# Performance work log

Measured on AMD Instinct MI355X. Metric: run time of the kernel, lower is better.

## Reference

```python
import jax, jax.numpy as jnp
import numpy as np
from jax import lax

EPS = 1e-5
K = 2


def conv1x1(x, w, b):
    # x: [B,C,H,W], w: [O,C], b: [O]
    return jnp.einsum('bchw,oc->bohw', x, w) + b[None, :, None, None]


def bn(x, g, b, m, v):
    # eval-mode BatchNorm2d with running stats m, v
    scale = g * lax.rsqrt(v + EPS)
    return (x - m[None, :, None, None]) * scale[None, :, None, None] + b[None, :, None, None]


def mrconv_xj(x, k):
    # Max-relative aggregation: running max over shifted diffs along H then W.
    # torch.cat([x[..,-i:,:], x[..,:-i,:]], dim=2) == roll by i along that axis.
    H, W = x.shape[2], x.shape[3]

    def make_step(axis):
        def step(xj, s):
            return jnp.maximum(xj, x - jnp.roll(x, s, axis=axis)), None
        return step

    shifts_h = jnp.arange(1, (H - 1) // k + 1) * k  # k, 2k, ..., < H
    shifts_w = jnp.arange(1, (W - 1) // k + 1) * k
    xj, _ = lax.scan(make_step(2), jnp.zeros_like(x), shifts_h)
    xj, _ = lax.scan(make_step(3), xj, shifts_w)
    return xj


def setup_inputs() -> dict:
    key = jax.random.key(0)
    ks = jax.random.split(key, 24)
    dim = 96
    B, H, W = 16, 112, 112
    d2, d4 = 2 * dim, 4 * dim

    def r(k, sh, s=0.05):
        return jax.random.normal(k, sh, jnp.float32) * s

    return dict(
        x=jax.random.normal(ks[0], (B, dim, H, W), jnp.float32),
        # Grapher.fc1: Conv2d(dim,dim,1) + BN(dim)
        w1=r(ks[1], (dim, dim)), b1=r(ks[2], (dim,)),
        g1=1.0 + r(ks[3], (dim,)), be1=r(ks[4], (dim,)),
        m1=r(ks[5], (dim,)), v1=1.0 + 0.1 * jax.random.uniform(ks[6], (dim,)),
        # MRConv4d.nn: Conv2d(2*dim, 2*dim, 1) + BN(2*dim) + GELU
        wg=r(ks[7], (d2, d2)), bg=r(ks[8], (d2,)),
        gg=1.0 + r(ks[9], (d2,)), beg=r(ks[10], (d2,)),
        mg=r(ks[11], (d2,)), vg=1.0 + 0.1 * jax.random.uniform(ks[12], (d2,)),
        # Grapher.fc2: Conv2d(2*dim, dim, 1) + BN(dim)
        w2=r(ks[13], (dim, d2)), b2=r(ks[14], (dim,)),
        g2=1.0 + r(ks[15], (dim,)), be2=r(ks[16], (dim,)),
        m2=r(ks[17], (dim,)), v2=1.0 + 0.1 * jax.random.uniform(ks[18], (dim,)),
        # FFN: Conv2d(dim, 4*dim, 1) -> GELU -> Conv2d(4*dim, dim, 1)
        wf1=r(ks[19], (d4, dim)), bf1=r(ks[20], (d4,)),
        wf2=r(ks[21], (dim, d4)), bf2=r(ks[22], (dim,)),
    )


def reference(x, w1, b1, g1, be1, m1, v1,
              wg, bg, gg, beg, mg, vg,
              w2, b2, g2, be2, m2, v2,
              wf1, bf1, wf2, bf2):
    # Grapher
    shortcut = x
    h = bn(conv1x1(x, w1, b1), g1, be1, m1, v1)          # fc1
    xj = mrconv_xj(h, K)                                 # max-relative graph conv
    h = jnp.concatenate([h, xj], axis=1)                 # [B, 2*dim, H, W]
    h = jax.nn.gelu(bn(conv1x1(h, wg, bg), gg, beg, mg, vg), approximate=False)
    h = bn(conv1x1(h, w2, b2), g2, be2, m2, v2) + shortcut  # fc2 + residual
    # FFN
    h = conv1x1(jax.nn.gelu(conv1x1(h, wf1, bf1), approximate=False), wf2, bf2)
    return h
```

## Files before the change

kernel.cpp:

```cpp
#include <hip/hip_runtime.h>
#include <hip/hip_bf16.h>
#include <math.h>

#define EPSC 1e-5f

typedef __attribute__((ext_vector_type(8))) short bf16x8;
typedef __attribute__((ext_vector_type(4))) float f32x4;
typedef __attribute__((ext_vector_type(8))) unsigned short u16x8;

constexpr int Bn = 16, Cn = 96, Hn = 112, Wn = 112, HWn = Hn * Wn;
constexpr int NT = 64, TPI = HWn / NT;

#define MFMA16(a, b, c) __builtin_amdgcn_mfma_f32_16x16x32_bf16((a), (b), (c), 0, 0, 0)

__device__ __forceinline__ ushort f2bf(float f) {
    __hip_bfloat16 h = __float2bfloat16(f);
    return __builtin_bit_cast(ushort, h);
}
__device__ __forceinline__ float bf2f(ushort u) {
    return __builtin_bit_cast(float, (unsigned)u << 16);
}
__device__ __forceinline__ float gelu_f(float x) {
    float t = x * x;
    float z = x * fmaf(0.0713548162726f, t, 1.59576912161f);
    float e = __expf(-z);
    return __fdividef(x, 1.0f + e);
}

__global__ __launch_bounds__(256) void params_kernel(
    const float* __restrict__ b1, const float* __restrict__ g1, const float* __restrict__ be1,
    const float* __restrict__ m1, const float* __restrict__ v1,
    const float* __restrict__ bg, const float* __restrict__ gg, const float* __restrict__ beg,
    const float* __restrict__ mg, const float* __restrict__ vg,
    const float* __restrict__ b2, const float* __restrict__ g2, const float* __restrict__ be2,
    const float* __restrict__ m2, const float* __restrict__ v2,
    float* __restrict__ P)
{
    int t = threadIdx.x;
    if (t < 96) {
        float s = g1[t] * rsqrtf(v1[t] + EPSC);
        P[t]       = s;
        P[96 + t]  = (b1[t] - m1[t]) * s + be1[t];
        float s2 = g2[t] * rsqrtf(v2[t] + EPSC);
        P[576 + t] = s2;
        P[672 + t] = (b2[t] - m2[t]) * s2 + be2[t];
    }
    if (t < 192) {
        float s = gg[t] * rsqrtf(vg[t] + EPSC);
        P[192 + t] = s;
        P[384 + t] = (bg[t] - mg[t]) * s + beg[t];
    }
}

__global__ __launch_bounds__(256) void pack_kernel(
    const float* __restrict__ w1, const float* __restrict__ wg, const float* __restrict__ w2,
    const float* __restrict__ wf1, const float* __restrict__ wf2,
    ushort* __restrict__ dst)
{
    int idx = blockIdx.x * 256 + threadIdx.x;
    if (idx >= 138240) return;
    const float* src; int K, off;
    if      (idx <   9216) { src = w1;  K =  96; off = 0;      }
    else if (idx <  46080) { src = wg;  K = 192; off = 9216;   }
    else if (idx <  64512) { src = w2;  K = 192; off = 46080;  }
    else if (idx < 101376) { src = wf1; K =  96; off = 64512;  }
    else                   { src = wf2; K = 384; off = 101376; }
    int r = idx - off;
    int e = r & 7, lane = (r >> 3) & 63, tile = r >> 9;
    int KC = K / 32;
    int kc = tile % KC, mt = tile / KC;
    int row = mt * 16 + (lane & 15);
    int col = kc * 32 + (lane >> 4) * 8 + e;
    dst[idx] = f2bf(src[(size_t)row * K + col]);
}

__global__ __launch_bounds__(256) void mins_kernel(
    const ushort* __restrict__ h, float* __restrict__ rmin2, float* __restrict__ cmin2)
{
    __shared__ __align__(16) ushort sl[112 * 96];
    int bid = blockIdx.x;
    int b = bid / 224, rem = bid % 224, mode = rem / 112, line = rem % 112;
    int t = threadIdx.x;
    if (mode == 0) {
        const ushort* base = h + ((size_t)b * HWn + line * Wn) * Cn;
        for (int v = t; v < 1344; v += 256)
            *(u16x8*)&sl[v * 8] = *(const u16x8*)&base[v * 8];
    } else {
        for (int v = t; v < 1344; v += 256) {
            int i = v / 12, g = v % 12;
            *(u16x8*)&sl[(i * 12 + g) * 8] =
                *(const u16x8*)&h[((size_t)b * HWn + i * Wn + line) * Cn + g * 8];
        }
    }
    __syncthreads();
    if (t < 192) {
        int c = t % 96, p = t / 96;
        float m = 1e30f;
        #pragma unroll 8
        for (int n = 0; n < 56; ++n) m = fminf(m, bf2f(sl[(p + 2 * n) * 96 + c]));
        float* dst = (mode == 0) ? rmin2 : cmin2;
        dst[(((size_t)b * 112 + line) * 2 + p) * 96 + c] = m;
    }
}

__global__ __launch_bounds__(256) void fc1_kernel(
    const float* __restrict__ X, const ushort* __restrict__ w1p,
    const float* __restrict__ prm, ushort* __restrict__ hbuf)
{
    __shared__ __align__(16) ushort Hs[64 * 104];
    int bid = blockIdx.x, b = bid / TPI, hw0 = (bid % TPI) * NT;
    int t = threadIdx.x, lane = t & 63, wave = t >> 6;
    int wm = wave >> 1, wn = wave & 1, q = lane >> 4, sl = lane & 15;

    bf16x8 bfr[3][2];
    #pragma unroll
    for (int kc = 0; kc < 3; ++kc)
        #pragma unroll
        for (int nc = 0; nc < 2; ++nc) {
            int s = hw0 + wn * 32 + nc * 16 + sl;
            union { bf16x8 v; ushort u[8]; } f;
            #pragma unroll
            for (int e = 0; e < 8; ++e) {
                int c = kc * 32 + q * 8 + e;
                f.u[e] = f2bf(X[((size_t)b * Cn + c) * HWn + s]);
            }
            bfr[kc][nc] = f.v;
        }
    f32x4 acc[3][2] = {};
    #pragma unroll
    for (int kc = 0; kc < 3; ++kc)
        #pragma unroll
        for (int m = 0; m < 3; ++m) {
            bf16x8 af = *(const bf16x8*)&w1p[(((wm * 3 + m) * 3 + kc) * 64 + lane) * 8];
            acc[m][0] = MFMA16(af, bfr[kc][0], acc[m][0]);
            acc[m][1] = MFMA16(af, bfr[kc][1], acc[m][1]);
        }
    #pragma unroll
    for (int m = 0; m < 3; ++m) {
        int o0 = (wm * 3 + m) * 16 + q * 4;
        f32x4 a4 = *(const f32x4*)&prm[o0];
        f32x4 s4 = *(const f32x4*)&prm[96 + o0];
        #pragma unroll
        for (int nc = 0; nc < 2; ++nc) {
            int srow = wn * 32 + nc * 16 + sl;
            ushort4 pk;
            pk.x = f2bf(acc[m][nc][0] * a4[0] + s4[0]);
            pk.y = f2bf(acc[m][nc][1] * a4[1] + s4[1]);
            pk.z = f2bf(acc[m][nc][2] * a4[2] + s4[2]);
            pk.w = f2bf(acc[m][nc][3] * a4[3] + s4[3]);
            *(ushort4*)&Hs[srow * 104 + o0] = pk;
        }
    }
    __syncthreads();
    for (int v = t; v < 768; v += 256) {
        int s = v / 12, g = v % 12;
        *(u16x8*)&hbuf[((size_t)b * HWn + hw0 + s) * Cn + g * 8] = *(const u16x8*)&Hs[s * 104 + g * 8];
    }
}

__global__ __launch_bounds__(256) void grapher_kernel(
    const ushort* __restrict__ hbuf, const float* __restrict__ Xres,
    const ushort* __restrict__ wgp, const ushort* __restrict__ w2p,
    const float* __restrict__ prm,
    const float* __restrict__ cmin2, const float* __restrict__ rmin2,
    ushort* __restrict__ rbuf)
{
    __shared__ __align__(16) ushort Xs[64 * 200];
    __shared__ __align__(16) ushort Gs[64 * 200];
    int bid = blockIdx.x, b = bid / TPI, hw0 = (bid % TPI) * NT;
    int t = threadIdx.x, lane = t & 63, wave = t >> 6;
    int wm = wave >> 1, wn = wave & 1, q = lane >> 4, sl = lane & 15;

    for (int v = t; v < 768; v += 256) {
        int s = v / 12, g = v % 12;
        u16x8 hv = *(const u16x8*)&hbuf[((size_t)b * HWn + hw0 + s) * Cn + g * 8];
        *(u16x8*)&Xs[s * 200 + g * 8] = hv;
        int pos = hw0 + s, i = pos / Wn, j = pos - i * Wn;
        const float* cm = &cmin2[(((size_t)b * 112 + j) * 2 + (i & 1)) * 96 + g * 8];
        const float* rm = &rmin2[(((size_t)b * 112 + i) * 2 + (j & 1)) * 96 + g * 8];
        union { u16x8 v; ushort u[8]; } hh, xx;
        hh.v = hv;
        #pragma unroll
        for (int e = 0; e < 8; ++e) {
            float hf = bf2f(hh.u[e]);
            xx.u[e] = f2bf(fmaxf(hf - cm[e], hf - rm[e]));
        }
        *(u16x8*)&Xs[s * 200 + 96 + g * 8] = xx.v;
    }
    __syncthreads();

    f32x4 acc[6][2] = {};
    #pragma unroll
    for (int kc = 0; kc < 6; ++kc) {
        bf16x8 b0 = *(const bf16x8*)&Xs[(wn * 32 + sl) * 200 + kc * 32 + q * 8];
        bf16x8 b1 = *(const bf16x8*)&Xs[(wn * 32 + 16 + sl) * 200 + kc * 32 + q * 8];
        #pragma unroll
        for (int m = 0; m < 6; ++m) {
            bf16x8 af = *(const bf16x8*)&wgp[(((wm * 6 + m) * 6 + kc) * 64 + lane) * 8];
            acc[m][0] = MFMA16(af, b0, acc[m][0]);
            acc[m][1] = MFMA16(af, b1, acc[m][1]);
        }
    }
    #pragma unroll
    for (int m = 0; m < 6; ++m) {
        int o0 = (wm * 6 + m) * 16 + q * 4;
        f32x4 a4 = *(const f32x4*)&prm[192 + o0];
        f32x4 s4 = *(const f32x4*)&prm[384 + o0];
        #pragma unroll
        for (int nc = 0; nc < 2; ++nc) {
            int srow = wn * 32 + nc * 16 + sl;
            ushort4 pk;
            pk.x = f2bf(gelu_f(acc[m][nc][0] * a4[0] + s4[0]));
            pk.y = f2bf(gelu_f(acc[m][nc][1] * a4[1] + s4[1]));
            pk.z = f2bf(gelu_f(acc[m][nc][2] * a4[2] + s4[2]));
            pk.w = f2bf(gelu_f(acc[m][nc][3] * a4[3] + s4[3]));
            *(ushort4*)&Gs[srow * 200 + o0] = pk;
        }
    }
    __syncthreads();

    f32x4 acc2[3][2] = {};
    #pragma unroll
    for (int kc = 0; kc < 6; ++kc) {
        bf16x8 b0 = *(const bf16x8*)&Gs[(wn * 32 + sl) * 200 + kc * 32 + q * 8];
        bf16x8 b1 = *(const bf16x8*)&Gs[(wn * 32 + 16 + sl) * 200 + kc * 32 + q * 8];
        #pragma unroll
        for (int m = 0; m < 3; ++m) {
            bf16x8 af = *(const bf16x8*)&w2p[(((wm * 3 + m) * 6 + kc) * 64 + lane) * 8];
            acc2[m][0] = MFMA16(af, b0, acc2[m][0]);
            acc2[m][1] = MFMA16(af, b1, acc2[m][1]);
        }
    }
    #pragma unroll
    for (int m = 0; m < 3; ++m) {
        int o0 = (wm * 3 + m) * 16 + q * 4;
        f32x4 a4 = *(const f32x4*)&prm[576 + o0];
        f32x4 s4 = *(const f32x4*)&prm[672 + o0];
        #pragma unroll
        for (int nc = 0; nc < 2; ++nc) {
            int srow = wn * 32 + nc * 16 + sl, sgl = hw0 + srow;
            ushort4 pk;
            float r0 = acc2[m][nc][0] * a4[0] + s4[0] + Xres[((size_t)b * Cn + o0 + 0) * HWn + sgl];
            float r1 = acc2[m][nc][1] * a4[1] + s4[1] + Xres[((size_t)b * Cn + o0 + 1) * HWn + sgl];
            float r2 = acc2[m][nc][2] * a4[2] + s4[2] + Xres[((size_t)b * Cn + o0 + 2) * HWn + sgl];
            float r3 = acc2[m][nc][3] * a4[3] + s4[3] + Xres[((size_t)b * Cn + o0 + 3) * HWn + sgl];
            pk.x = f2bf(r0); pk.y = f2bf(r1); pk.z = f2bf(r2); pk.w = f2bf(r3);
            *(ushort4*)&Xs[srow * 200 + o0] = pk;
        }
    }
    __syncthreads();
    for (int v = t; v < 768; v += 256) {
        int s = v / 12, g = v % 12;
        *(u16x8*)&rbuf[((size_t)b * HWn + hw0 + s) * Cn + g * 8] = *(const u16x8*)&Xs[s * 200 + g * 8];
    }
}

__global__ __launch_bounds__(256) void ffn_kernel(
    const ushort* __restrict__ rbuf,
    const ushort* __restrict__ wf1p, const float* __restrict__ bf1,
    const ushort* __restrict__ wf2p, const float* __restrict__ bf2,
    float* __restrict__ Out)
{
    __shared__ __align__(16) ushort Rs[64 * 104];
    __shared__ __align__(16) ushort Mc[2][64 * 104];
    int bid = blockIdx.x, b = bid / TPI, hw0 = (bid % TPI) * NT;
    int t = threadIdx.x, lane = t & 63, wave = t >> 6;
    int wm = wave >> 1, wn = wave & 1, q = lane >> 4, sl = lane & 15;

    for (int v = t; v < 768; v += 256) {
        int s = v / 12, g = v % 12;
        *(u16x8*)&Rs[s * 104 + g * 8] = *(const u16x8*)&rbuf[((size_t)b * HWn + hw0 + s) * Cn + g * 8];
    }
    __syncthreads();

    bf16x8 rb[3][2];
    #pragma unroll
    for (int kc = 0; kc < 3; ++kc) {
        rb[kc][0] = *(const bf16x8*)&Rs[(wn * 32 + sl) * 104 + kc * 32 + q * 8];
        rb[kc][1] = *(const bf16x8*)&Rs[(wn * 32 + 16 + sl) * 104 + kc * 32 + q * 8];
    }

    f32x4 acc2[3][2] = {};
    for (int c = 0; c < 4; ++c) {
        f32x4 a1[3][2] = {};
        #pragma unroll
        for (int kc = 0; kc < 3; ++kc)
            #pragma unroll
            for (int m = 0; m < 3; ++m) {
                bf16x8 af = *(const bf16x8*)&wf1p[(((c * 6 + wm * 3 + m) * 3 + kc) * 64 + lane) * 8];
                a1[m][0] = MFMA16(af, rb[kc][0], a1[m][0]);
                a1[m][1] = MFMA16(af, rb[kc][1], a1[m][1]);
            }
        ushort* mc = (ushort*)Mc[c & 1];
        #pragma unroll
        for (int m = 0; m < 3; ++m) {
            int ol = (wm * 3 + m) * 16 + q * 4;
            f32x4 b4 = *(const f32x4*)&bf1[c * 96 + ol];
            #pragma unroll
            for (int nc = 0; nc < 2; ++nc) {
                int srow = wn * 32 + nc * 16 + sl;
                ushort4 pk;
                pk.x = f2bf(gelu_f(a1[m][nc][0] + b4[0]));
                pk.y = f2bf(gelu_f(a1[m][nc][1] + b4[1]));
                pk.z = f2bf(gelu_f(a1[m][nc][2] + b4[2]));
                pk.w = f2bf(gelu_f(a1[m][nc][3] + b4[3]));
                *(ushort4*)&mc[srow * 104 + ol] = pk;
            }
        }
        __syncthreads();
        #pragma unroll
        for (int kc = 0; kc < 3; ++kc) {
            bf16x8 m0 = *(const bf16x8*)&mc[(wn * 32 + sl) * 104 + kc * 32 + q * 8];
            bf16x8 m1 = *(const bf16x8*)&mc[(wn * 32 + 16 + sl) * 104 + kc * 32 + q * 8];
            #pragma unroll
            for (int m = 0; m < 3; ++m) {
                bf16x8 af = *(const bf16x8*)&wf2p[(((wm * 3 + m) * 12 + c * 3 + kc) * 64 + lane) * 8];
                acc2[m][0] = MFMA16(af, m0, acc2[m][0]);
                acc2[m][1] = MFMA16(af, m1, acc2[m][1]);
            }
        }
    }
    #pragma unroll
    for (int m = 0; m < 3; ++m) {
        int o0 = (wm * 3 + m) * 16 + q * 4;
        f32x4 b4 = *(const f32x4*)&bf2[o0];
        #pragma unroll
        for (int nc = 0; nc < 2; ++nc) {
            int sgl = hw0 + wn * 32 + nc * 16 + sl;
            Out[((size_t)b * Cn + o0 + 0) * HWn + sgl] = acc2[m][nc][0] + b4[0];
            Out[((size_t)b * Cn + o0 + 1) * HWn + sgl] = acc2[m][nc][1] + b4[1];
            Out[((size_t)b * Cn + o0 + 2) * HWn + sgl] = acc2[m][nc][2] + b4[2];
            Out[((size_t)b * Cn + o0 + 3) * HWn + sgl] = acc2[m][nc][3] + b4[3];
        }
    }
}

extern "C" void kernel_launch(void* const* d_in, const int* in_sizes, int n_in,
                              void* d_out, int out_size, void* d_ws, size_t ws_size,
                              hipStream_t stream) {
    (void)in_sizes; (void)n_in; (void)out_size; (void)ws_size;
    const float* x   = (const float*)d_in[0];
    const float* w1  = (const float*)d_in[1];
    const float* b1  = (const float*)d_in[2];
    const float* g1  = (const float*)d_in[3];
    const float* be1 = (const float*)d_in[4];
    const float* m1  = (const float*)d_in[5];
    const float* v1  = (const float*)d_in[6];
    const float* wg  = (const float*)d_in[7];
    const float* bg  = (const float*)d_in[8];
    const float* gg  = (const float*)d_in[9];
    const float* beg = (const float*)d_in[10];
    const float* mg  = (const float*)d_in[11];
    const float* vg  = (const float*)d_in[12];
    const float* w2  = (const float*)d_in[13];
    const float* b2  = (const float*)d_in[14];
    const float* g2  = (const float*)d_in[15];
    const float* be2 = (const float*)d_in[16];
    const float* m2  = (const float*)d_in[17];
    const float* v2  = (const float*)d_in[18];
    const float* wf1 = (const float*)d_in[19];
    const float* bf1 = (const float*)d_in[20];
    const float* wf2 = (const float*)d_in[21];
    const float* bf2 = (const float*)d_in[22];
    float* out = (float*)d_out;

    char* base = (char*)d_ws;
    const size_t H_BYTES   = (size_t)Bn * HWn * Cn * 2;
    const size_t MIN_BYTES = (size_t)Bn * 112 * 2 * 96 * 4;
    ushort* hbuf  = (ushort*)base;
    float*  rmin2 = (float*)(base + H_BYTES);
    float*  cmin2 = (float*)(base + H_BYTES + MIN_BYTES);
    float*  prm   = (float*)(base + H_BYTES + 2 * MIN_BYTES);
    ushort* wpack = (ushort*)(base + H_BYTES + 2 * MIN_BYTES + 3072);
    ushort* w1p  = wpack;
    ushort* wgp  = wpack + 9216;
    ushort* w2p  = wpack + 46080;
    ushort* wf1p = wpack + 64512;
    ushort* wf2p = wpack + 101376;

    params_kernel<<<dim3(1), dim3(256), 0, stream>>>(
        b1, g1, be1, m1, v1, bg, gg, beg, mg, vg, b2, g2, be2, m2, v2, prm);
    pack_kernel<<<dim3(540), dim3(256), 0, stream>>>(w1, wg, w2, wf1, wf2, wpack);

    dim3 grid(Bn * TPI), blk(256);
    fc1_kernel<<<grid, blk, 0, stream>>>(x, w1p, prm, hbuf);
    mins_kernel<<<dim3(Bn * 2 * 112), blk, 0, stream>>>(hbuf, rmin2, cmin2);
    grapher_kernel<<<grid, blk, 0, stream>>>(hbuf, x, wgp, w2p, prm, cmin2, rmin2, hbuf);
    ffn_kernel<<<grid, blk, 0, stream>>>(hbuf, wf1p, bf1, wf2p, bf2, out);
}
```

Measured before the change: 211.5 us.

## Fuse grapher and FFN into one register-resident kernel with permuted weight packing

Merges grapher_kernel and ffn_kernel into a single mega_kernel in which each wave owns 16 spatial positions. Intermediate activations stay in registers: the MFMA accumulator outputs are repacked directly as B operands for the next matmul instead of going through LDS. To make that work, the w2, wf1 and wf2 packing is permuted along K so it matches the accumulator register layout. This removes the rbuf global round trip, the LDS staging and the __syncthreads, at the cost of more register pressure and per-wave reloading of the full weight fragments from global/L2, with launch_bounds set to 4 blocks.

```diff
diff --git a/kernel.cpp b/kernel.cpp
--- a/kernel.cpp
+++ b/kernel.cpp
@@ -25,6 +25,9 @@
     float z = x * fmaf(0.0713548162726f, t, 1.59576912161f);
     float e = __expf(-z);
     return __fdividef(x, 1.0f + e);
+}
+__device__ __forceinline__ uint pk2(float lo, float hi) {
+    return (uint)f2bf(lo) | ((uint)f2bf(hi) << 16);
 }
 
 __global__ __launch_bounds__(256) void params_kernel(
@@ -59,18 +62,20 @@
 {
     int idx = blockIdx.x * 256 + threadIdx.x;
     if (idx >= 138240) return;
-    const float* src; int K, off;
-    if      (idx <   9216) { src = w1;  K =  96; off = 0;      }
-    else if (idx <  46080) { src = wg;  K = 192; off = 9216;   }
-    else if (idx <  64512) { src = w2;  K = 192; off = 46080;  }
-    else if (idx < 101376) { src = wf1; K =  96; off = 64512;  }
-    else                   { src = wf2; K = 384; off = 101376; }
+    const float* src; int K, off; bool perm;
+    if      (idx <   9216) { src = w1;  K =  96; off = 0;      perm = false; }
+    else if (idx <  46080) { src = wg;  K = 192; off = 9216;   perm = false; }
+    else if (idx <  64512) { src = w2;  K = 192; off = 46080;  perm = true;  }
+    else if (idx < 101376) { src = wf1; K =  96; off = 64512;  perm = true;  }
+    else                   { src = wf2; K = 384; off = 101376; perm = true;  }
     int r = idx - off;
     int e = r & 7, lane = (r >> 3) & 63, tile = r >> 9;
     int KC = K / 32;
     int kc = tile % KC, mt = tile / KC;
     int row = mt * 16 + (lane & 15);
-    int col = kc * 32 + (lane >> 4) * 8 + e;
+    int col;
+    if (!perm) col = kc * 32 + (lane >> 4) * 8 + e;
+    else       col = ((kc >> 1) * 4 + (kc & 1) * 2 + (e >> 2)) * 16 + (lane >> 4) * 4 + (e & 3);
     dst[idx] = f2bf(src[(size_t)row * K + col]);
 }
 
@@ -158,180 +163,136 @@
     }
 }
 
-__global__ __launch_bounds__(256) void grapher_kernel(
+__global__ __launch_bounds__(256, 4) void mega_kernel(
     const ushort* __restrict__ hbuf, const float* __restrict__ Xres,
     const ushort* __restrict__ wgp, const ushort* __restrict__ w2p,
-    const float* __restrict__ prm,
+    const ushort* __restrict__ wf1p, const ushort* __restrict__ wf2p,
+    const float* __restrict__ prm, const float* __restrict__ bf1,
+    const float* __restrict__ bf2,
     const float* __restrict__ cmin2, const float* __restrict__ rmin2,
-    ushort* __restrict__ rbuf)
-{
-    __shared__ __align__(16) ushort Xs[64 * 200];
-    __shared__ __align__(16) ushort Gs[64 * 200];
+    float* __restrict__ Out)
+{
     int bid = blockIdx.x, b = bid / TPI, hw0 = (bid % TPI) * NT;
-    int t = threadIdx.x, lane = t & 63, wave = t >> 6;
-    int wm = wave >> 1, wn = wave & 1, q = lane >> 4, sl = lane & 15;
-
-    for (int v = t; v < 768; v += 256) {
-        int s = v / 12, g = v % 12;
-        u16x8 hv = *(const u16x8*)&hbuf[((size_t)b * HWn + hw0 + s) * Cn + g * 8];
-        *(u16x8*)&Xs[s * 200 + g * 8] = hv;
-        int pos = hw0 + s, i = pos / Wn, j = pos - i * Wn;
-        const float* cm = &cmin2[(((size_t)b * 112 + j) * 2 + (i & 1)) * 96 + g * 8];
-        const float* rm = &rmin2[(((size_t)b * 112 + i) * 2 + (j & 1)) * 96 + g * 8];
-        union { u16x8 v; ushort u[8]; } hh, xx;
-        hh.v = hv;
-        #pragma unroll
-        for (int e = 0; e < 8; ++e) {
-            float hf = bf2f(hh.u[e]);
-            xx.u[e] = f2bf(fmaxf(hf - cm[e], hf - rm[e]));
-        }
-        *(u16x8*)&Xs[s * 200 + 96 + g * 8] = xx.v;
-    }
-    __syncthreads();
-
-    f32x4 acc[6][2] = {};
+    int t = threadIdx.x, lane = t & 63, wv = t >> 6, q = lane >> 4, sl = lane & 15;
+    const int s = hw0 + wv * 16 + sl;
+    const int i = s / Wn, j = s - i * Wn;
+
+    union U8 { bf16x8 v; ushort u[8]; uint d[4]; };
+    const ushort* hrow = hbuf + ((size_t)b * HWn + s) * 96;
+    const size_t cmb = (((size_t)b * 112 + j) * 2 + (i & 1)) * 96;
+    const size_t rmb = (((size_t)b * 112 + i) * 2 + (j & 1)) * 96;
+
+    U8 cb[6];
+    #pragma unroll
+    for (int kc = 0; kc < 3; ++kc)
+        cb[kc].v = *(const bf16x8*)&hrow[kc * 32 + q * 8];
+    #pragma unroll
+    for (int kc = 0; kc < 3; ++kc) {
+        int c0 = kc * 32 + q * 8;
+        f32x4 cma = *(const f32x4*)&cmin2[cmb + c0];
+        f32x4 cmb2 = *(const f32x4*)&cmin2[cmb + c0 + 4];
+        f32x4 rma = *(const f32x4*)&rmin2[rmb + c0];
+        f32x4 rmb2 = *(const f32x4*)&rmin2[rmb + c0 + 4];
+        U8 xx;
+        #pragma unroll
+        for (int e = 0; e < 4; ++e) {
+            float hf = bf2f(cb[kc].u[e]);
+            xx.u[e] = f2bf(fmaxf(hf - cma[e], hf - rma[e]));
+        }
+        #pragma unroll
+        for (int e = 0; e < 4; ++e) {
+            float hf = bf2f(cb[kc].u[4 + e]);
+            xx.u[4 + e] = f2bf(fmaxf(hf - cmb2[e], hf - rmb2[e]));
+        }
+        cb[3 + kc] = xx;
+    }
+
+    f32x4 ga[12] = {};
+    #pragma unroll
+    for (int kc = 0; kc < 6; ++kc)
+        #pragma unroll
+        for (int m = 0; m < 12; ++m) {
+            bf16x8 af = *(const bf16x8*)&wgp[((m * 6 + kc) * 64 + lane) * 8];
+            ga[m] = MFMA16(af, cb[kc].v, ga[m]);
+        }
+    uint gpk[12][2];
+    #pragma unroll
+    for (int m = 0; m < 12; ++m) {
+        int t0 = m * 16 + q * 4;
+        f32x4 a4 = *(const f32x4*)&prm[192 + t0];
+        f32x4 s4 = *(const f32x4*)&prm[384 + t0];
+        gpk[m][0] = pk2(gelu_f(ga[m][0] * a4[0] + s4[0]), gelu_f(ga[m][1] * a4[1] + s4[1]));
+        gpk[m][1] = pk2(gelu_f(ga[m][2] * a4[2] + s4[2]), gelu_f(ga[m][3] * a4[3] + s4[3]));
+    }
+
+    f32x4 r2[6] = {};
     #pragma unroll
     for (int kc = 0; kc < 6; ++kc) {
-        bf16x8 b0 = *(const bf16x8*)&Xs[(wn * 32 + sl) * 200 + kc * 32 + q * 8];
-        bf16x8 b1 = *(const bf16x8*)&Xs[(wn * 32 + 16 + sl) * 200 + kc * 32 + q * 8];
+        int M = (kc >> 1) * 4 + (kc & 1) * 2;
+        U8 gb;
+        gb.d[0] = gpk[M][0];     gb.d[1] = gpk[M][1];
+        gb.d[2] = gpk[M + 1][0]; gb.d[3] = gpk[M + 1][1];
         #pragma unroll
         for (int m = 0; m < 6; ++m) {
-            bf16x8 af = *(const bf16x8*)&wgp[(((wm * 6 + m) * 6 + kc) * 64 + lane) * 8];
-            acc[m][0] = MFMA16(af, b0, acc[m][0]);
-            acc[m][1] = MFMA16(af, b1, acc[m][1]);
-        }
-    }
+            bf16x8 af = *(const bf16x8*)&w2p[((m * 6 + kc) * 64 + lane) * 8];
+            r2[m] = MFMA16(af, gb.v, r2[m]);
+        }
+    }
+    uint rpk[6][2];
     #pragma unroll
     for (int m = 0; m < 6; ++m) {
-        int o0 = (wm * 6 + m) * 16 + q * 4;
-        f32x4 a4 = *(const f32x4*)&prm[192 + o0];
-        f32x4 s4 = *(const f32x4*)&prm[384 + o0];
-        #pragma unroll
-        for (int nc = 0; nc < 2; ++nc) {
-            int srow = wn * 32 + nc * 16 + sl;
-            ushort4 pk;
-            pk.x = f2bf(gelu_f(acc[m][nc][0] * a4[0] + s4[0]));
-            pk.y = f2bf(gelu_f(acc[m][nc][1] * a4[1] + s4[1]));
-            pk.z = f2bf(gelu_f(acc[m][nc][2] * a4[2] + s4[2]));
-            pk.w = f2bf(gelu_f(acc[m][nc][3] * a4[3] + s4[3]));
-            *(ushort4*)&Gs[srow * 200 + o0] = pk;
-        }
-    }
-    __syncthreads();
-
-    f32x4 acc2[3][2] = {};
-    #pragma unroll
-    for (int kc = 0; kc < 6; ++kc) {
-        bf16x8 b0 = *(const bf16x8*)&Gs[(wn * 32 + sl) * 200 + kc * 32 + q * 8];
-        bf16x8 b1 = *(const bf16x8*)&Gs[(wn * 32 + 16 + sl) * 200 + kc * 32 + q * 8];
-        #pragma unroll
-        for (int m = 0; m < 3; ++m) {
-            bf16x8 af = *(const bf16x8*)&w2p[(((wm * 3 + m) * 6 + kc) * 64 + lane) * 8];
-            acc2[m][0] = MFMA16(af, b0, acc2[m][0]);
-            acc2[m][1] = MFMA16(af, b1, acc2[m][1]);
-        }
-    }
-    #pragma unroll
-    for (int m = 0; m < 3; ++m) {
-        int o0 = (wm * 3 + m) * 16 + q * 4;
-        f32x4 a4 = *(const f32x4*)&prm[576 + o0];
-        f32x4 s4 = *(const f32x4*)&prm[672 + o0];
-        #pragma unroll
-        for (int nc = 0; nc < 2; ++nc) {
-            int srow = wn * 32 + nc * 16 + sl, sgl = hw0 + srow;
-            ushort4 pk;
-            float r0 = acc2[m][nc][0] * a4[0] + s4[0] + Xres[((size_t)b * Cn + o0 + 0) * HWn + sgl];
-            float r1 = acc2[m][nc][1] * a4[1] + s4[1] + Xres[((size_t)b * Cn + o0 + 1) * HWn + sgl];
-            float r2 = acc2[m][nc][2] * a4[2] + s4[2] + Xres[((size_t)b * Cn + o0 + 2) * HWn + sgl];
-            float r3 = acc2[m][nc][3] * a4[3] + s4[3] + Xres[((size_t)b * Cn + o0 + 3) * HWn + sgl];
-            pk.x = f2bf(r0); pk.y = f2bf(r1); pk.z = f2bf(r2); pk.w = f2bf(r3);
-            *(ushort4*)&Xs[srow * 200 + o0] = pk;
-        }
-    }
-    __syncthreads();
-    for (int v = t; v < 768; v += 256) {
-        int s = v / 12, g = v % 12;
-        *(u16x8*)&rbuf[((size_t)b * HWn + hw0 + s) * Cn + g * 8] = *(const u16x8*)&Xs[s * 200 + g * 8];
-    }
-}
-
-__global__ __launch_bounds__(256) void ffn_kernel(
-    const ushort* __restrict__ rbuf,
-    const ushort* __restrict__ wf1p, const float* __restrict__ bf1,
-    const ushort* __restrict__ wf2p, const float* __restrict__ bf2,
-    float* __restrict__ Out)
-{
-    __shared__ __align__(16) ushort Rs[64 * 104];
-    __shared__ __align__(16) ushort Mc[2][64 * 104];
-    int bid = blockIdx.x, b = bid / TPI, hw0 = (bid % TPI) * NT;
-    int t = threadIdx.x, lane = t & 63, wave = t >> 6;
-    int wm = wave >> 1, wn = wave & 1, q = lane >> 4, sl = lane & 15;
-
-    for (int v = t; v < 768; v += 256) {
-        int s = v / 12, g = v % 12;
-        *(u16x8*)&Rs[s * 104 + g * 8] = *(const u16x8*)&rbuf[((size_t)b * HWn + hw0 + s) * Cn + g * 8];
-    }
-    __syncthreads();
-
-    bf16x8 rb[3][2];
+        int t0 = m * 16 + q * 4;
+        f32x4 a4 = *(const f32x4*)&prm[576 + t0];
+        f32x4 s4 = *(const f32x4*)&prm[672 + t0];
+        float rv[4];
+        #pragma unroll
+        for (int r = 0; r < 4; ++r)
+            rv[r] = r2[m][r] * a4[r] + s4[r] + Xres[((size_t)b * 96 + t0 + r) * HWn + s];
+        rpk[m][0] = pk2(rv[0], rv[1]);
+        rpk[m][1] = pk2(rv[2], rv[3]);
+    }
+    U8 rB[3];
     #pragma unroll
     for (int kc = 0; kc < 3; ++kc) {
-        rb[kc][0] = *(const bf16x8*)&Rs[(wn * 32 + sl) * 104 + kc * 32 + q * 8];
-        rb[kc][1] = *(const bf16x8*)&Rs[(wn * 32 + 16 + sl) * 104 + kc * 32 + q * 8];
-    }
-
-    f32x4 acc2[3][2] = {};
-    for (int c = 0; c < 4; ++c) {
-        f32x4 a1[3][2] = {};
+        rB[kc].d[0] = rpk[kc * 2][0];     rB[kc].d[1] = rpk[kc * 2][1];
+        rB[kc].d[2] = rpk[kc * 2 + 1][0]; rB[kc].d[3] = rpk[kc * 2 + 1][1];
+    }
+
+    f32x4 oacc[6] = {};
+    for (int c = 0; c < 6; ++c) {
+        f32x4 a1[4] = {};
         #pragma unroll
         for (int kc = 0; kc < 3; ++kc)
             #pragma unroll
-            for (int m = 0; m < 3; ++m) {
-                bf16x8 af = *(const bf16x8*)&wf1p[(((c * 6 + wm * 3 + m) * 3 + kc) * 64 + lane) * 8];
-                a1[m][0] = MFMA16(af, rb[kc][0], a1[m][0]);
-                a1[m][1] = MFMA16(af, rb[kc][1], a1[m][1]);
+            for (int m = 0; m < 4; ++m) {
+                bf16x8 af = *(const bf16x8*)&wf1p[(((c * 4 + m) * 3 + kc) * 64 + lane) * 8];
+                a1[m] = MFMA16(af, rB[kc].v, a1[m]);
             }
-        ushort* mc = (ushort*)Mc[c & 1];
-        #pragma unroll
-        for (int m = 0; m < 3; ++m) {
-            int ol = (wm * 3 + m) * 16 + q * 4;
-            f32x4 b4 = *(const f32x4*)&bf1[c * 96 + ol];
-            #pragma unroll
-            for (int nc = 0; nc < 2; ++nc) {
-                int srow = wn * 32 + nc * 16 + sl;
-                ushort4 pk;
-                pk.x = f2bf(gelu_f(a1[m][nc][0] + b4[0]));
-                pk.y = f2bf(gelu_f(a1[m][nc][1] + b4[1]));
-                pk.z = f2bf(gelu_f(a1[m][nc][2] + b4[2]));
-                pk.w = f2bf(gelu_f(a1[m][nc][3] + b4[3]));
-                *(ushort4*)&mc[srow * 104 + ol] = pk;
-            }
-        }
-        __syncthreads();
-        #pragma unroll
-        for (int kc = 0; kc < 3; ++kc) {
-            bf16x8 m0 = *(const bf16x8*)&mc[(wn * 32 + sl) * 104 + kc * 32 + q * 8];
-            bf16x8 m1 = *(const bf16x8*)&mc[(wn * 32 + 16 + sl) * 104 + kc * 32 + q * 8];
-            #pragma unroll
-            for (int m = 0; m < 3; ++m) {
-                bf16x8 af = *(const bf16x8*)&wf2p[(((wm * 3 + m) * 12 + c * 3 + kc) * 64 + lane) * 8];
-                acc2[m][0] = MFMA16(af, m0, acc2[m][0]);
-                acc2[m][1] = MFMA16(af, m1, acc2[m][1]);
-            }
-        }
-    }
-    #pragma unroll
-    for (int m = 0; m < 3; ++m) {
-        int o0 = (wm * 3 + m) * 16 + q * 4;
-        f32x4 b4 = *(const f32x4*)&bf2[o0];
-        #pragma unroll
-        for (int nc = 0; nc < 2; ++nc) {
-            int sgl = hw0 + wn * 32 + nc * 16 + sl;
-            Out[((size_t)b * Cn + o0 + 0) * HWn + sgl] = acc2[m][nc][0] + b4[0];
-            Out[((size_t)b * Cn + o0 + 1) * HWn + sgl] = acc2[m][nc][1] + b4[1];
-            Out[((size_t)b * Cn + o0 + 2) * HWn + sgl] = acc2[m][nc][2] + b4[2];
-            Out[((size_t)b * Cn + o0 + 3) * HWn + sgl] = acc2[m][nc][3] + b4[3];
-        }
+        uint mpk[4][2];
+        #pragma unroll
+        for (int m = 0; m < 4; ++m) {
+            f32x4 b4 = *(const f32x4*)&bf1[(c * 4 + m) * 16 + q * 4];
+            mpk[m][0] = pk2(gelu_f(a1[m][0] + b4[0]), gelu_f(a1[m][1] + b4[1]));
+            mpk[m][1] = pk2(gelu_f(a1[m][2] + b4[2]), gelu_f(a1[m][3] + b4[3]));
+        }
+        U8 mB0, mB1;
+        mB0.d[0] = mpk[0][0]; mB0.d[1] = mpk[0][1]; mB0.d[2] = mpk[1][0]; mB0.d[3] = mpk[1][1];
+        mB1.d[0] = mpk[2][0]; mB1.d[1] = mpk[2][1]; mB1.d[2] = mpk[3][0]; mB1.d[3] = mpk[3][1];
+        #pragma unroll
+        for (int m = 0; m < 6; ++m) {
+            bf16x8 af0 = *(const bf16x8*)&wf2p[((m * 12 + c * 2) * 64 + lane) * 8];
+            oacc[m] = MFMA16(af0, mB0.v, oacc[m]);
+            bf16x8 af1 = *(const bf16x8*)&wf2p[((m * 12 + c * 2 + 1) * 64 + lane) * 8];
+            oacc[m] = MFMA16(af1, mB1.v, oacc[m]);
+        }
+    }
+    #pragma unroll
+    for (int m = 0; m < 6; ++m) {
+        int t0 = m * 16 + q * 4;
+        f32x4 b4 = *(const f32x4*)&bf2[t0];
+        #pragma unroll
+        for (int r = 0; r < 4; ++r)
+            Out[((size_t)b * 96 + t0 + r) * HWn + s] = oacc[m][r] + b4[r];
     }
 }
 
@@ -385,6 +346,6 @@
     dim3 grid(Bn * TPI), blk(256);
     fc1_kernel<<<grid, blk, 0, stream>>>(x, w1p, prm, hbuf);
     mins_kernel<<<dim3(Bn * 2 * 112), blk, 0, stream>>>(hbuf, rmin2, cmin2);
-    grapher_kernel<<<grid, blk, 0, stream>>>(hbuf, x, wgp, w2p, prm, cmin2, rmin2, hbuf);
-    ffn_kernel<<<grid, blk, 0, stream>>>(hbuf, wf1p, bf1, wf2p, bf2, out);
-}
+    mega_kernel<<<grid, blk, 0, stream>>>(hbuf, x, wgp, w2p, wf1p, wf2p,
+                                          prm, bf1, bf2, cmin2, rmin2, out);
+}
```

Result: slower. 309.9 us (+46.5%).

## Fuse grapher and FFN kernels into one tail kernel sharing LDS

Applied to the files above, without the earlier changes.

Merges the grapher kernel (graph conv, fc2 and residual) and the FFN kernel into a single kernel. The residual tile stays in shared memory and feeds the FFN directly instead of going to global memory as bf16 and being reloaded. Shared memory is reused: Xs holds the residual and Gs is split into the FFN double buffers. This saves one launch and a full activation write plus read, but raises per-block register pressure and lengthens the kernel.

```diff
diff --git a/kernel.cpp b/kernel.cpp
--- a/kernel.cpp
+++ b/kernel.cpp
@@ -158,15 +158,19 @@
     }
 }
 
-__global__ __launch_bounds__(256) void grapher_kernel(
+__global__ __launch_bounds__(256) void tail_kernel(
     const ushort* __restrict__ hbuf, const float* __restrict__ Xres,
     const ushort* __restrict__ wgp, const ushort* __restrict__ w2p,
+    const ushort* __restrict__ wf1p, const float* __restrict__ bf1,
+    const ushort* __restrict__ wf2p, const float* __restrict__ bf2,
     const float* __restrict__ prm,
     const float* __restrict__ cmin2, const float* __restrict__ rmin2,
-    ushort* __restrict__ rbuf)
-{
-    __shared__ __align__(16) ushort Xs[64 * 200];
-    __shared__ __align__(16) ushort Gs[64 * 200];
+    float* __restrict__ Out)
+{
+    __shared__ __align__(16) ushort S[26112];
+    ushort* Xs = S;
+    ushort* Gs = S + 12800;
+
     int bid = blockIdx.x, b = bid / TPI, hw0 = (bid % TPI) * NT;
     int t = threadIdx.x, lane = t & 63, wave = t >> 6;
     int wm = wave >> 1, wn = wave & 1, q = lane >> 4, sl = lane & 15;
@@ -189,95 +193,76 @@
     }
     __syncthreads();
 
-    f32x4 acc[6][2] = {};
-    #pragma unroll
-    for (int kc = 0; kc < 6; ++kc) {
-        bf16x8 b0 = *(const bf16x8*)&Xs[(wn * 32 + sl) * 200 + kc * 32 + q * 8];
-        bf16x8 b1 = *(const bf16x8*)&Xs[(wn * 32 + 16 + sl) * 200 + kc * 32 + q * 8];
+    {
+        f32x4 acc[6][2] = {};
+        #pragma unroll
+        for (int kc = 0; kc < 6; ++kc) {
+            bf16x8 b0 = *(const bf16x8*)&Xs[(wn * 32 + sl) * 200 + kc * 32 + q * 8];
+            bf16x8 b1 = *(const bf16x8*)&Xs[(wn * 32 + 16 + sl) * 200 + kc * 32 + q * 8];
+            #pragma unroll
+            for (int m = 0; m < 6; ++m) {
+                bf16x8 af = *(const bf16x8*)&wgp[(((wm * 6 + m) * 6 + kc) * 64 + lane) * 8];
+                acc[m][0] = MFMA16(af, b0, acc[m][0]);
+                acc[m][1] = MFMA16(af, b1, acc[m][1]);
+            }
+        }
         #pragma unroll
         for (int m = 0; m < 6; ++m) {
-            bf16x8 af = *(const bf16x8*)&wgp[(((wm * 6 + m) * 6 + kc) * 64 + lane) * 8];
-            acc[m][0] = MFMA16(af, b0, acc[m][0]);
-            acc[m][1] = MFMA16(af, b1, acc[m][1]);
-        }
-    }
-    #pragma unroll
-    for (int m = 0; m < 6; ++m) {
-        int o0 = (wm * 6 + m) * 16 + q * 4;
-        f32x4 a4 = *(const f32x4*)&prm[192 + o0];
-        f32x4 s4 = *(const f32x4*)&prm[384 + o0];
-        #pragma unroll
-        for (int nc = 0; nc < 2; ++nc) {
-            int srow = wn * 32 + nc * 16 + sl;
-            ushort4 pk;
-            pk.x = f2bf(gelu_f(acc[m][nc][0] * a4[0] + s4[0]));
-            pk.y = f2bf(gelu_f(acc[m][nc][1] * a4[1] + s4[1]));
-            pk.z = f2bf(gelu_f(acc[m][nc][2] * a4[2] + s4[2]));
-            pk.w = f2bf(gelu_f(acc[m][nc][3] * a4[3] + s4[3]));
-            *(ushort4*)&Gs[srow * 200 + o0] = pk;
-        }
-    }
-    __syncthreads();
-
-    f32x4 acc2[3][2] = {};
-    #pragma unroll
-    for (int kc = 0; kc < 6; ++kc) {
-        bf16x8 b0 = *(const bf16x8*)&Gs[(wn * 32 + sl) * 200 + kc * 32 + q * 8];
-        bf16x8 b1 = *(const bf16x8*)&Gs[(wn * 32 + 16 + sl) * 200 + kc * 32 + q * 8];
+            int o0 = (wm * 6 + m) * 16 + q * 4;
+            f32x4 a4 = *(const f32x4*)&prm[192 + o0];
+            f32x4 s4 = *(const f32x4*)&prm[384 + o0];
+            #pragma unroll
+            for (int nc = 0; nc < 2; ++nc) {
+                int srow = wn * 32 + nc * 16 + sl;
+                ushort4 pk;
+                pk.x = f2bf(gelu_f(acc[m][nc][0] * a4[0] + s4[0]));
+                pk.y = f2bf(gelu_f(acc[m][nc][1] * a4[1] + s4[1]));
+                pk.z = f2bf(gelu_f(acc[m][nc][2] * a4[2] + s4[2]));
+                pk.w = f2bf(gelu_f(acc[m][nc][3] * a4[3] + s4[3]));
+                *(ushort4*)&Gs[srow * 200 + o0] = pk;
+            }
+        }
+    }
+    __syncthreads();
+
+    {
+        f32x4 acc2[3][2] = {};
+        #pragma unroll
+        for (int kc = 0; kc < 6; ++kc) {
+            bf16x8 b0 = *(const bf16x8*)&Gs[(wn * 32 + sl) * 200 + kc * 32 + q * 8];
+            bf16x8 b1 = *(const bf16x8*)&Gs[(wn * 32 + 16 + sl) * 200 + kc * 32 + q * 8];
+            #pragma unroll
+            for (int m = 0; m < 3; ++m) {
+                bf16x8 af = *(const bf16x8*)&w2p[(((wm * 3 + m) * 6 + kc) * 64 + lane) * 8];
+                acc2[m][0] = MFMA16(af, b0, acc2[m][0]);
+                acc2[m][1] = MFMA16(af, b1, acc2[m][1]);
+            }
+        }
         #pragma unroll
         for (int m = 0; m < 3; ++m) {
-            bf16x8 af = *(const bf16x8*)&w2p[(((wm * 3 + m) * 6 + kc) * 64 + lane) * 8];
-            acc2[m][0] = MFMA16(af, b0, acc2[m][0]);
-            acc2[m][1] = MFMA16(af, b1, acc2[m][1]);
-        }
-    }
-    #pragma unroll
-    for (int m = 0; m < 3; ++m) {
-        int o0 = (wm * 3 + m) * 16 + q * 4;
-        f32x4 a4 = *(const f32x4*)&prm[576 + o0];
-        f32x4 s4 = *(const f32x4*)&prm[672 + o0];
-        #pragma unroll
-        for (int nc = 0; nc < 2; ++nc) {
-            int srow = wn * 32 + nc * 16 + sl, sgl = hw0 + srow;
-            ushort4 pk;
-            float r0 = acc2[m][nc][0] * a4[0] + s4[0] + Xres[((size_t)b * Cn + o0 + 0) * HWn + sgl];
-            float r1 = acc2[m][nc][1] * a4[1] + s4[1] + Xres[((size_t)b * Cn + o0 + 1) * HWn + sgl];
-            float r2 = acc2[m][nc][2] * a4[2] + s4[2] + Xres[((size_t)b * Cn + o0 + 2) * HWn + sgl];
-            float r3 = acc2[m][nc][3] * a4[3] + s4[3] + Xres[((size_t)b * Cn + o0 + 3) * HWn + sgl];
-            pk.x = f2bf(r0); pk.y = f2bf(r1); pk.z = f2bf(r2); pk.w = f2bf(r3);
-            *(ushort4*)&Xs[srow * 200 + o0] = pk;
-        }
-    }
-    __syncthreads();
-    for (int v = t; v < 768; v += 256) {
-        int s = v / 12, g = v % 12;
-        *(u16x8*)&rbuf[((size_t)b * HWn + hw0 + s) * Cn + g * 8] = *(const u16x8*)&Xs[s * 200 + g * 8];
-    }
-}
-
-__global__ __launch_bounds__(256) void ffn_kernel(
-    const ushort* __restrict__ rbuf,
-    const ushort* __restrict__ wf1p, const float* __restrict__ bf1,
-    const ushort* __restrict__ wf2p, const float* __restrict__ bf2,
-    float* __restrict__ Out)
-{
-    __shared__ __align__(16) ushort Rs[64 * 104];
-    __shared__ __align__(16) ushort Mc[2][64 * 104];
-    int bid = blockIdx.x, b = bid / TPI, hw0 = (bid % TPI) * NT;
-    int t = threadIdx.x, lane = t & 63, wave = t >> 6;
-    int wm = wave >> 1, wn = wave & 1, q = lane >> 4, sl = lane & 15;
-
-    for (int v = t; v < 768; v += 256) {
-        int s = v / 12, g = v % 12;
-        *(u16x8*)&Rs[s * 104 + g * 8] = *(const u16x8*)&rbuf[((size_t)b * HWn + hw0 + s) * Cn + g * 8];
+            int o0 = (wm * 3 + m) * 16 + q * 4;
+            f32x4 a4 = *(const f32x4*)&prm[576 + o0];
+            f32x4 s4 = *(const f32x4*)&prm[672 + o0];
+            #pragma unroll
+            for (int nc = 0; nc < 2; ++nc) {
+                int srow = wn * 32 + nc * 16 + sl, sgl = hw0 + srow;
+                ushort4 pk;
+                float r0 = acc2[m][nc][0] * a4[0] + s4[0] + Xres[((size_t)b * Cn + o0 + 0) * HWn + sgl];
+                float r1 = acc2[m][nc][1] * a4[1] + s4[1] + Xres[((size_t)b * Cn + o0 + 1) * HWn + sgl];
+                float r2 = acc2[m][nc][2] * a4[2] + s4[2] + Xres[((size_t)b * Cn + o0 + 2) * HWn + sgl];
+                float r3 = acc2[m][nc][3] * a4[3] + s4[3] + Xres[((size_t)b * Cn + o0 + 3) * HWn + sgl];
+                pk.x = f2bf(r0); pk.y = f2bf(r1); pk.z = f2bf(r2); pk.w = f2bf(r3);
+                *(ushort4*)&Xs[srow * 200 + o0] = pk;
+            }
+        }
     }
     __syncthreads();
 
     bf16x8 rb[3][2];
     #pragma unroll
     for (int kc = 0; kc < 3; ++kc) {
-        rb[kc][0] = *(const bf16x8*)&Rs[(wn * 32 + sl) * 104 + kc * 32 + q * 8];
-        rb[kc][1] = *(const bf16x8*)&Rs[(wn * 32 + 16 + sl) * 104 + kc * 32 + q * 8];
+        rb[kc][0] = *(const bf16x8*)&Xs[(wn * 32 + sl) * 200 + kc * 32 + q * 8];
+        rb[kc][1] = *(const bf16x8*)&Xs[(wn * 32 + 16 + sl) * 200 + kc * 32 + q * 8];
     }
 
     f32x4 acc2[3][2] = {};
@@ -291,7 +276,7 @@
                 a1[m][0] = MFMA16(af, rb[kc][0], a1[m][0]);
                 a1[m][1] = MFMA16(af, rb[kc][1], a1[m][1]);
             }
-        ushort* mc = (ushort*)Mc[c & 1];
+        ushort* mc = Gs + (c & 1) * 6656;
         #pragma unroll
         for (int m = 0; m < 3; ++m) {
             int ol = (wm * 3 + m) * 16 + q * 4;
@@ -382,9 +367,10 @@
         b1, g1, be1, m1, v1, bg, gg, beg, mg, vg, b2, g2, be2, m2, v2, prm);
     pack_kernel<<<dim3(540), dim3(256), 0, stream>>>(w1, wg, w2, wf1, wf2, wpack);
 
-    dim3 grid(Bn * TPI), blk(256);
-    fc1_kernel<<<grid, blk, 0, stream>>>(x, w1p, prm, hbuf);
+    dim3 blk(256);
+    fc1_kernel<<<dim3(Bn * TPI), blk, 0, stream>>>(x, w1p, prm, hbuf);
     mins_kernel<<<dim3(Bn * 2 * 112), blk, 0, stream>>>(hbuf, rmin2, cmin2);
-    grapher_kernel<<<grid, blk, 0, stream>>>(hbuf, x, wgp, w2p, prm, cmin2, rmin2, hbuf);
-    ffn_kernel<<<grid, blk, 0, stream>>>(hbuf, wf1p, bf1, wf2p, bf2, out);
-}
+    tail_kernel<<<dim3(Bn * TPI), blk, 0, stream>>>(hbuf, x, wgp, w2p,
+                                                    wf1p, bf1, wf2p, bf2,
+                                                    prm, cmin2, rmin2, out);
+}
```

After: 289.6 us. +36.9%, slower.
